# Kernel tuning notes

Measured on AMD Instinct MI355X. Metric: run time of the kernel, lower is better.

## Reference

```python
import jax, jax.numpy as jnp
import numpy as np

K = 16            # neighbors
RATIO = 0.25      # sampling ratio
BN_EPS = 1e-5


def setup_inputs() -> dict:
    key = jax.random.key(0)
    k1, k2, k3 = jax.random.split(key, 3)
    B, N, Cin, Cout = 8, 8192, 64, 128
    x = jax.random.normal(k1, (B, N, Cin), dtype=jnp.float32)
    p1 = jax.random.uniform(k2, (B, N, 3), dtype=jnp.float32)
    W = jax.random.normal(k3, (Cout, Cin), dtype=jnp.float32) * 0.05  # Conv1d(k=1, bias=False)
    gamma = jnp.ones((Cout,), dtype=jnp.float32)   # BatchNorm1d weight
    beta = jnp.zeros((Cout,), dtype=jnp.float32)   # BatchNorm1d bias
    return {"x": x, "p1": p1, "W": W, "gamma": gamma, "beta": beta}


def furthest_point_sample(p, M):
    """Greedy FPS. p: (B,N,3) -> (B,M) int32 indices. Starts at index 0 (CUDA impl convention)."""
    B, N, _ = p.shape
    first = jnp.zeros((B,), dtype=jnp.int32)
    mind = jnp.full((B, N), 1e10, dtype=p.dtype)

    def step(carry, _):
        mind, last = carry
        lp = jnp.take_along_axis(p, last[:, None, None].astype(jnp.int32), axis=1)  # (B,1,3)
        d = jnp.sum((p - lp) ** 2, axis=-1)          # (B,N)
        mind = jnp.minimum(mind, d)
        nxt = jnp.argmax(mind, axis=1).astype(jnp.int32)
        return (mind, nxt), nxt

    (_, _), rest = jax.lax.scan(step, (mind, first), None, length=M - 1)  # rest: (M-1,B)
    idx = jnp.concatenate([first[None, :], rest], axis=0)  # (M,B)
    return idx.T  # (B,M)


def reference(x, p1, W, gamma, beta):
    B, N, Cin = x.shape
    M = int(N * RATIO)

    # --- FPS sampling + gather coords ---
    fps_idx = furthest_point_sample(p1, M)                      # (B,M)
    p2 = jnp.take_along_axis(p1, fps_idx[:, :, None], axis=1)   # (B,M,3)

    # --- brute-force kNN of p1 around each p2 query ---
    d2 = (jnp.sum(p2 ** 2, -1)[:, :, None]
          - 2.0 * jnp.einsum('bmd,bnd->bmn', p2, p1)
          + jnp.sum(p1 ** 2, -1)[:, None, :])                   # (B,M,N)
    _, nbr = jax.lax.top_k(-d2, K)                              # (B,M,K) indices into N

    # --- shared MLP: 1x1 conv (no bias) + BatchNorm1d (training-mode stats) + ReLU ---
    h = jnp.einsum('bnc,oc->bno', x, W)                         # (B,N,Cout)
    mean = jnp.mean(h, axis=(0, 1))
    var = jnp.var(h, axis=(0, 1))
    h = (h - mean) * jax.lax.rsqrt(var + BN_EPS) * gamma + beta
    h = jax.nn.relu(h)

    # --- gather k neighbors per sampled point, max-pool over neighborhood ---
    feats = h[jnp.arange(B)[:, None, None], nbr]                # (B,M,K,Cout)
    y = jnp.max(feats, axis=2)                                  # (B,M,Cout)
    return y, p2
```

## Files before the change

kernel.cpp:

```cpp
#include <hip/hip_runtime.h>
#include <stdint.h>

#define Bb   8
#define Nn   8192
#define CIN  64
#define COUT 128
#define Mm   2048
#define KNN  16
#define NTOT (Bb*Nn)

typedef unsigned long long ull;
typedef float v2f __attribute__((ext_vector_type(2)));

#define MAGIC 0x55AA1234u


__device__ __forceinline__ v2f pk_add(v2f a, v2f b)
{ v2f d; asm("v_pk_add_f32 %0, %1, %2" : "=v"(d) : "v"(a), "v"(b)); return d; }
__device__ __forceinline__ v2f pk_mul(v2f a, v2f b)
{ v2f d; asm("v_pk_mul_f32 %0, %1, %2" : "=v"(d) : "v"(a), "v"(b)); return d; }

__device__ __forceinline__ float wave_max16(float x)
{
    int v = __float_as_int(x), t;
    t = __builtin_amdgcn_update_dpp(v, v, 0x111, 0xf, 0xf, false);
    v = __float_as_int(fmaxf(__int_as_float(v), __int_as_float(t)));
    t = __builtin_amdgcn_update_dpp(v, v, 0x112, 0xf, 0xf, false);
    v = __float_as_int(fmaxf(__int_as_float(v), __int_as_float(t)));
    t = __builtin_amdgcn_update_dpp(v, v, 0x114, 0xf, 0xf, false);
    v = __float_as_int(fmaxf(__int_as_float(v), __int_as_float(t)));
    t = __builtin_amdgcn_update_dpp(v, v, 0x118, 0xf, 0xf, false);
    v = __float_as_int(fmaxf(__int_as_float(v), __int_as_float(t)));
    unsigned r0 = (unsigned)__builtin_amdgcn_readlane(v, 15);
    unsigned r1 = (unsigned)__builtin_amdgcn_readlane(v, 31);
    unsigned r2 = (unsigned)__builtin_amdgcn_readlane(v, 47);
    unsigned r3 = (unsigned)__builtin_amdgcn_readlane(v, 63);
    unsigned m0 = r0 > r1 ? r0 : r1;
    unsigned m1 = r2 > r3 ? r2 : r3;
    unsigned mm = m0 > m1 ? m0 : m1;
    return __uint_as_float(mm);
}

__device__ __forceinline__ ull d2key(
    float qx, float qy, float qz, float qn, float x, float y, float z, int j)
{
    float dot = __fadd_rn(__fadd_rn(__fmul_rn(qx, x), __fmul_rn(qy, y)),
                          __fmul_rn(qz, z));
    float cn  = __fadd_rn(__fadd_rn(__fmul_rn(x, x), __fmul_rn(y, y)),
                          __fmul_rn(z, z));
    float d2  = __fadd_rn(__fsub_rn(qn, __fadd_rn(dot, dot)), cn);
    unsigned int bits = __float_as_uint(d2);
    unsigned int u = bits ^ (((unsigned int)((int)bits >> 31)) | 0x80000000u);
    return ((ull)u << 32) | (unsigned int)j;
}

__global__ __launch_bounds__(256, 1)
void mega_kernel(const float* __restrict__ p1, float* __restrict__ p2out,
                 const float* __restrict__ h, const float* __restrict__ sb,
                 ull* idxpub, float* __restrict__ y)
{
    __shared__ float px[Nn], py[Nn], pz[Nn];
    __shared__ alignas(16) ull wkey[2][4];
    const int tid = threadIdx.x;

    if (blockIdx.x < 8) {
        const int b    = blockIdx.x;
        const int lane = tid & 63, wid = tid >> 6;
        const float* pb = p1 + b * Nn * 3;

        for (int i = tid; i < Nn * 3; i += 256) {
            float v = pb[i];
            int pt = i / 3;
            int c  = i - pt * 3;
            if (c == 0) px[pt] = v; else if (c == 1) py[pt] = v; else pz[pt] = v;
        }
        __syncthreads();

        v2f ppx[16], ppy[16], ppz[16], mind[16];
#pragma unroll
        for (int i = 0; i < 16; ++i) {
            int j0 = tid * 32 + 2 * i;
            ppx[i] = (v2f){px[j0], px[j0 + 1]};
            ppy[i] = (v2f){py[j0], py[j0 + 1]};
            ppz[i] = (v2f){pz[j0], pz[j0 + 1]};
            mind[i] = (v2f){1e10f, 1e10f};
        }

        float lx = px[0], ly = py[0], lz = pz[0];
        if (tid == 0) {
            __hip_atomic_store(&idxpub[b * Mm], ((ull)MAGIC << 32) | 0ull,
                               __ATOMIC_RELAXED, __HIP_MEMORY_SCOPE_AGENT);
            int o = (b * Mm) * 3;
            p2out[o] = lx; p2out[o + 1] = ly; p2out[o + 2] = lz;
        }

        for (int m = 1; m < Mm; ++m) {
            const int buf = m & 1;
            float nx = -lx, ny = -ly, nz = -lz;
            v2f nx2 = (v2f){nx, nx}, ny2 = (v2f){ny, ny}, nz2 = (v2f){nz, nz};
            float bv0 = -1.0f, bv1 = -1.0f; int bj0 = 0, bj1 = 1;
#pragma unroll
            for (int i = 0; i < 16; ++i) {
                v2f dx = pk_add(ppx[i], nx2);
                v2f dy = pk_add(ppy[i], ny2);
                v2f dz = pk_add(ppz[i], nz2);
                v2f s  = pk_add(pk_add(pk_mul(dx, dx), pk_mul(dy, dy)),
                                pk_mul(dz, dz));
                float m0 = fminf(mind[i].x, s.x);
                float m1 = fminf(mind[i].y, s.y);
                mind[i].x = m0; mind[i].y = m1;
                if (m0 > bv0) { bv0 = m0; bj0 = 2 * i; }
                if (m1 > bv1) { bv1 = m1; bj1 = 2 * i + 1; }
            }
            float bestv; int bestj;
            if (bv1 > bv0 || (bv1 == bv0 && bj1 < bj0)) { bestv = bv1; bestj = bj1; }
            else                                        { bestv = bv0; bestj = bj0; }
            bestj += tid * 32;

            float wv = wave_max16(bestv);
            ull tie = __ballot(bestv == wv);
            int low = __ffsll((long long)tie) - 1;
            if (lane == low) {
                wkey[buf][wid] = ((ull)__float_as_uint(wv) << 32) |
                                 (unsigned int)(~(unsigned int)bestj);
            }
            __syncthreads();

            ull k0 = wkey[buf][0], k1 = wkey[buf][1];
            ull k2 = wkey[buf][2], k3 = wkey[buf][3];
            ull k01 = k0 > k1 ? k0 : k1;
            ull k23 = k2 > k3 ? k2 : k3;
            ull fk  = k01 > k23 ? k01 : k23;
            int jw = (int)(~(unsigned int)fk);
            if (tid == 0) {
                __hip_atomic_store(&idxpub[b * Mm + m],
                                   ((ull)MAGIC << 32) | (ull)(unsigned)jw,
                                   __ATOMIC_RELAXED, __HIP_MEMORY_SCOPE_AGENT);
            }
            lx = px[jw]; ly = py[jw]; lz = pz[jw];
            if (tid == 0) {
                int o = (b * Mm + m) * 3;
                p2out[o] = lx; p2out[o + 1] = ly; p2out[o + 2] = lz;
            }
        }
        return;
    }

    const int cb = blockIdx.x - 8;
    const int b  = cb / 31;
    const int k  = cb - b * 31;
    const float* pb = p1 + b * Nn * 3;

    for (int i = tid; i < Nn * 3; i += 256) {
        float v = pb[i];
        int pt = i / 3;
        int c  = i - pt * 3;
        if (c == 0) px[pt] = v; else if (c == 1) py[pt] = v; else pz[pt] = v;
    }
    __syncthreads();

    const int w = tid >> 6, lane = tid & 63;
    const int c0 = lane * 2;
    const float s0 = sb[c0], s1 = sb[c0 + 1];
    const float bb0 = sb[128 + c0], bb1 = sb[128 + c0 + 1];
    const ull INV = ~0ull;

    for (int t = w; k + 31 * t < Mm; t += 4) {
        const int m = k + 31 * t;
        const int qrow = b * Mm + m;

        ull pv;
        for (;;) {
            pv = __hip_atomic_load(&idxpub[qrow], __ATOMIC_RELAXED,
                                   __HIP_MEMORY_SCOPE_AGENT);
            if ((unsigned)(pv >> 32) == MAGIC) break;
            __builtin_amdgcn_s_sleep(2);
        }
        const int jq = (int)(pv & 0x1FFFull);
        const float qx = px[jq], qy = py[jq], qz = pz[jq];
        const float qn = __fadd_rn(__fadd_rn(__fmul_rn(qx, qx), __fmul_rn(qy, qy)),
                                   __fmul_rn(qz, qz));

        ull k1 = INV, k2 = INV, k3 = INV;
#pragma unroll 4
        for (int i = 0; i < 128; ++i) {
            int j = lane + (i << 6);
            ull key = d2key(qx, qy, qz, qn, px[j], py[j], pz[j], j);
            bool b1 = key < k1, b2 = key < k2, b3 = key < k3;
            ull n1 = b1 ? key : k1;
            ull n2 = b1 ? k1 : (b2 ? key : k2);
            ull n3 = b2 ? k2 : (b3 ? key : k3);
            k1 = n1; k2 = n2; k3 = n3;
        }

        float a0 = -1e30f, a1 = -1e30f;
        for (int r = 0; r < KNN; ++r) {
            ull wk = k1;
#pragma unroll
            for (int off = 1; off < 64; off <<= 1) {
                ull ok = __shfl_xor(wk, off, 64);
                wk = ok < wk ? ok : wk;
            }
            const int n = (int)(unsigned int)(wk & 0xFFFFFFFFull);
            const float2 v = *(const float2*)(h + (((b << 13) + n) * COUT) + c0);
            if (k1 == wk) { k1 = k2; k2 = k3; k3 = INV; }
            if (k1 == INV) {
                for (int i = 0; i < 128; ++i) {
                    int j = lane + (i << 6);
                    ull key = d2key(qx, qy, qz, qn, px[j], py[j], pz[j], j);
                    if (key > wk) {
                        bool b1 = key < k1, b2 = key < k2, b3 = key < k3;
                        ull n1 = b1 ? key : k1;
                        ull n2 = b1 ? k1 : (b2 ? key : k2);
                        ull n3 = b2 ? k2 : (b3 ? key : k3);
                        k1 = n1; k2 = n2; k3 = n3;
                    }
                }
            }
            a0 = fmaxf(a0, fmaf(v.x, s0, bb0));
            a1 = fmaxf(a1, fmaf(v.y, s1, bb1));
        }
        a0 = fmaxf(a0, 0.0f); a1 = fmaxf(a1, 0.0f);
        *(float2*)(y + qrow * COUT + c0) = make_float2(a0, a1);
    }
}

__global__ __launch_bounds__(256)
void gemm_kernel(const float* __restrict__ x, const float* __restrict__ W,
                 float* __restrict__ h)
{
    const int r0 = blockIdx.x * 16 + (threadIdx.x >> 6) * 4;
    const int cp = threadIdx.x & 63;
    const float4* xp = (const float4*)(x + r0 * CIN);
    const float4* w0 = (const float4*)(W + (cp * 2) * CIN);
    const float4* w1 = (const float4*)(W + (cp * 2 + 1) * CIN);
    float a[4][2];
#pragma unroll
    for (int r = 0; r < 4; ++r) { a[r][0] = 0.f; a[r][1] = 0.f; }
#pragma unroll
    for (int k = 0; k < CIN / 4; ++k) {
        float4 wa = w0[k], wb = w1[k];
#pragma unroll
        for (int r = 0; r < 4; ++r) {
            float4 xv = xp[r * 16 + k];
            a[r][0] = fmaf(xv.x, wa.x, fmaf(xv.y, wa.y, fmaf(xv.z, wa.z, fmaf(xv.w, wa.w, a[r][0]))));
            a[r][1] = fmaf(xv.x, wb.x, fmaf(xv.y, wb.y, fmaf(xv.z, wb.z, fmaf(xv.w, wb.w, a[r][1]))));
        }
    }
#pragma unroll
    for (int r = 0; r < 4; ++r)
        *(float2*)(h + (r0 + r) * COUT + cp * 2) = make_float2(a[r][0], a[r][1]);
}

__global__ __launch_bounds__(256)
void stats_kernel(const float* __restrict__ h, float* __restrict__ stats)
{
    __shared__ float4 rs[256], rq[256];
    const int tid  = threadIdx.x;
    const int c4   = (tid & 31) * 4;
    const int rsub = tid >> 5;
    const int rbase = blockIdx.x * 256;
    float4 s = make_float4(0, 0, 0, 0), q = make_float4(0, 0, 0, 0);
    for (int i = 0; i < 32; ++i) {
        int r = rbase + rsub + i * 8;
        float4 v = *(const float4*)(h + r * COUT + c4);
        s.x += v.x; s.y += v.y; s.z += v.z; s.w += v.w;
        q.x = fmaf(v.x, v.x, q.x); q.y = fmaf(v.y, v.y, q.y);
        q.z = fmaf(v.z, v.z, q.z); q.w = fmaf(v.w, v.w, q.w);
    }
    rs[tid] = s; rq[tid] = q;
    __syncthreads();
    if (tid < 32) {
        for (int j = 1; j < 8; ++j) {
            float4 o = rs[tid + 32 * j];
            s.x += o.x; s.y += o.y; s.z += o.z; s.w += o.w;
            float4 oq = rq[tid + 32 * j];
            q.x += oq.x; q.y += oq.y; q.z += oq.z; q.w += oq.w;
        }
        atomicAdd(&stats[c4 + 0], s.x); atomicAdd(&stats[c4 + 1], s.y);
        atomicAdd(&stats[c4 + 2], s.z); atomicAdd(&stats[c4 + 3], s.w);
        atomicAdd(&stats[128 + c4 + 0], q.x); atomicAdd(&stats[128 + c4 + 1], q.y);
        atomicAdd(&stats[128 + c4 + 2], q.z); atomicAdd(&stats[128 + c4 + 3], q.w);
    }
}

__global__ void finalize_kernel(const float* __restrict__ stats,
                                const float* __restrict__ gamma,
                                const float* __restrict__ beta,
                                float* __restrict__ sb)
{
    int c = threadIdx.x;
    float mean = stats[c] * (1.0f / 65536.0f);
    float var  = stats[128 + c] * (1.0f / 65536.0f) - mean * mean;
    float scale = gamma[c] / sqrtf(var + 1e-5f);
    float bias  = beta[c] - mean * scale;
    sb[c] = scale; sb[128 + c] = bias;
}

extern "C" void kernel_launch(void* const* d_in, const int* in_sizes, int n_in,
                              void* d_out, int out_size, void* d_ws, size_t ws_size,
                              hipStream_t stream)
{
    const float* x     = (const float*)d_in[0];
    const float* p1    = (const float*)d_in[1];
    const float* W     = (const float*)d_in[2];
    const float* gamma = (const float*)d_in[3];
    const float* beta  = (const float*)d_in[4];

    float* y  = (float*)d_out;
    float* p2 = (float*)d_out + Bb * Mm * COUT;

    char*  ws     = (char*)d_ws;
    float* h      = (float*)ws;
    ull*   idxpub = (ull*)(ws + 33619968);
    float* stats  = (float*)(ws + 35717120);
    float* sb     = (float*)(ws + 35718144);

    hipMemsetAsync(stats, 0, 1024, stream);
    gemm_kernel<<<NTOT / 16, 256, 0, stream>>>(x, W, h);
    stats_kernel<<<256, 256, 0, stream>>>(h, stats);
    finalize_kernel<<<1, 128, 0, stream>>>(stats, gamma, beta, sb);
    mega_kernel<<<256, 256, 0, stream>>>(p1, p2, h, sb, idxpub, y);
}
```

Before: 2.097 ms.

## Fuse GEMM, BN stats and finalize into persistent mega kernel; double block size

Moves the 1x1-conv GEMM and the BatchNorm statistics into the consumer blocks of the persistent mega kernel, where they run while the FPS blocks start sampling. A grid-wide atomic counter barrier makes those blocks wait until all statistics are accumulated. Block size goes from 256 to 512 threads, so each FPS thread handles 16 points instead of 32 and the kNN blocks run 8 waves. This removes three kernel launches and the serial GEMM+stats prefix ahead of FPS. In exchange it relies on all 256 blocks being co-resident for the spin barrier, and the wider FPS block has a larger cross-wave reduction on every step.

```diff
diff --git a/kernel.cpp b/kernel.cpp
--- a/kernel.cpp
+++ b/kernel.cpp
@@ -8,6 +8,7 @@
 #define Mm   2048
 #define KNN  16
 #define NTOT (Bb*Nn)
+#define NCONS 248
 
 typedef unsigned long long ull;
 typedef float v2f __attribute__((ext_vector_type(2)));
@@ -54,21 +55,23 @@
     return ((ull)u << 32) | (unsigned int)j;
 }
 
-__global__ __launch_bounds__(256, 1)
+__global__ __launch_bounds__(512, 1)
 void mega_kernel(const float* __restrict__ p1, float* __restrict__ p2out,
-                 const float* __restrict__ h, const float* __restrict__ sb,
-                 ull* idxpub, float* __restrict__ y)
+                 const float* __restrict__ x, const float* __restrict__ W,
+                 const float* __restrict__ gamma, const float* __restrict__ beta,
+                 float* __restrict__ h, float* __restrict__ stats,
+                 unsigned int* done, ull* idxpub, float* __restrict__ y)
 {
     __shared__ float px[Nn], py[Nn], pz[Nn];
-    __shared__ alignas(16) ull wkey[2][4];
+    __shared__ alignas(16) ull wkey[2][8];
     const int tid = threadIdx.x;
+    const int w = tid >> 6, lane = tid & 63;
 
     if (blockIdx.x < 8) {
-        const int b    = blockIdx.x;
-        const int lane = tid & 63, wid = tid >> 6;
+        const int b = blockIdx.x;
         const float* pb = p1 + b * Nn * 3;
 
-        for (int i = tid; i < Nn * 3; i += 256) {
+        for (int i = tid; i < Nn * 3; i += 512) {
             float v = pb[i];
             int pt = i / 3;
             int c  = i - pt * 3;
@@ -76,10 +79,10 @@
         }
         __syncthreads();
 
-        v2f ppx[16], ppy[16], ppz[16], mind[16];
-#pragma unroll
-        for (int i = 0; i < 16; ++i) {
-            int j0 = tid * 32 + 2 * i;
+        v2f ppx[8], ppy[8], ppz[8], mind[8];
+#pragma unroll
+        for (int i = 0; i < 8; ++i) {
+            int j0 = tid * 16 + 2 * i;
             ppx[i] = (v2f){px[j0], px[j0 + 1]};
             ppy[i] = (v2f){py[j0], py[j0 + 1]};
             ppz[i] = (v2f){pz[j0], pz[j0 + 1]};
@@ -100,7 +103,7 @@
             v2f nx2 = (v2f){nx, nx}, ny2 = (v2f){ny, ny}, nz2 = (v2f){nz, nz};
             float bv0 = -1.0f, bv1 = -1.0f; int bj0 = 0, bj1 = 1;
 #pragma unroll
-            for (int i = 0; i < 16; ++i) {
+            for (int i = 0; i < 8; ++i) {
                 v2f dx = pk_add(ppx[i], nx2);
                 v2f dy = pk_add(ppy[i], ny2);
                 v2f dz = pk_add(ppz[i], nz2);
@@ -115,22 +118,20 @@
             float bestv; int bestj;
             if (bv1 > bv0 || (bv1 == bv0 && bj1 < bj0)) { bestv = bv1; bestj = bj1; }
             else                                        { bestv = bv0; bestj = bj0; }
-            bestj += tid * 32;
+            bestj += tid * 16;
 
             float wv = wave_max16(bestv);
             ull tie = __ballot(bestv == wv);
             int low = __ffsll((long long)tie) - 1;
             if (lane == low) {
-                wkey[buf][wid] = ((ull)__float_as_uint(wv) << 32) |
-                                 (unsigned int)(~(unsigned int)bestj);
+                wkey[buf][w] = ((ull)__float_as_uint(wv) << 32) |
+                               (unsigned int)(~(unsigned int)bestj);
             }
             __syncthreads();
 
-            ull k0 = wkey[buf][0], k1 = wkey[buf][1];
-            ull k2 = wkey[buf][2], k3 = wkey[buf][3];
-            ull k01 = k0 > k1 ? k0 : k1;
-            ull k23 = k2 > k3 ? k2 : k3;
-            ull fk  = k01 > k23 ? k01 : k23;
+            ull fk = wkey[buf][0];
+#pragma unroll
+            for (int q = 1; q < 8; ++q) { ull k = wkey[buf][q]; fk = k > fk ? k : fk; }
             int jw = (int)(~(unsigned int)fk);
             if (tid == 0) {
                 __hip_atomic_store(&idxpub[b * Mm + m],
@@ -147,11 +148,74 @@
     }
 
     const int cb = blockIdx.x - 8;
-    const int b  = cb / 31;
-    const int k  = cb - b * 31;
+    const int cp = lane;
+    {
+        const float4* w0 = (const float4*)(W + (cp * 2) * CIN);
+        const float4* w1 = (const float4*)(W + (cp * 2 + 1) * CIN);
+        float s0 = 0.f, s1 = 0.f, q0 = 0.f, q1 = 0.f;
+        for (int r0 = cb * 32 + w * 4; r0 < NTOT; r0 += NCONS * 32) {
+            const float4* xp = (const float4*)(x + r0 * CIN);
+            float a[4][2];
+#pragma unroll
+            for (int r = 0; r < 4; ++r) { a[r][0] = 0.f; a[r][1] = 0.f; }
+#pragma unroll
+            for (int k = 0; k < CIN / 4; ++k) {
+                float4 wa = w0[k], wb = w1[k];
+#pragma unroll
+                for (int r = 0; r < 4; ++r) {
+                    float4 xv = xp[r * 16 + k];
+                    a[r][0] = fmaf(xv.x, wa.x, fmaf(xv.y, wa.y, fmaf(xv.z, wa.z, fmaf(xv.w, wa.w, a[r][0]))));
+                    a[r][1] = fmaf(xv.x, wb.x, fmaf(xv.y, wb.y, fmaf(xv.z, wb.z, fmaf(xv.w, wb.w, a[r][1]))));
+                }
+            }
+#pragma unroll
+            for (int r = 0; r < 4; ++r) {
+                *(float2*)(h + (r0 + r) * COUT + cp * 2) = make_float2(a[r][0], a[r][1]);
+                s0 += a[r][0]; s1 += a[r][1];
+                q0 = fmaf(a[r][0], a[r][0], q0); q1 = fmaf(a[r][1], a[r][1], q1);
+            }
+        }
+        float4* comb = (float4*)px;
+        comb[w * 64 + cp] = make_float4(s0, s1, q0, q1);
+        __syncthreads();
+        if (tid < 64) {
+            float4 t = comb[cp];
+#pragma unroll
+            for (int j = 1; j < 8; ++j) {
+                float4 o = comb[j * 64 + cp];
+                t.x += o.x; t.y += o.y; t.z += o.z; t.w += o.w;
+            }
+            atomicAdd(&stats[2 * cp], t.x);     atomicAdd(&stats[2 * cp + 1], t.y);
+            atomicAdd(&stats[128 + 2 * cp], t.z); atomicAdd(&stats[128 + 2 * cp + 1], t.w);
+        }
+        __syncthreads();
+        if (tid == 0) {
+            __hip_atomic_fetch_add(done, 1u, __ATOMIC_RELEASE,
+                                   __HIP_MEMORY_SCOPE_AGENT);
+            while (__hip_atomic_load(done, __ATOMIC_ACQUIRE,
+                                     __HIP_MEMORY_SCOPE_AGENT) < NCONS)
+                __builtin_amdgcn_s_sleep(2);
+        }
+        __syncthreads();
+    }
+
+    float sc0, sc1, bi0, bi1;
+    {
+        float mean0 = stats[2 * cp] * (1.0f / 65536.0f);
+        float mean1 = stats[2 * cp + 1] * (1.0f / 65536.0f);
+        float var0  = stats[128 + 2 * cp] * (1.0f / 65536.0f) - mean0 * mean0;
+        float var1  = stats[128 + 2 * cp + 1] * (1.0f / 65536.0f) - mean1 * mean1;
+        sc0 = gamma[2 * cp] / sqrtf(var0 + 1e-5f);
+        sc1 = gamma[2 * cp + 1] / sqrtf(var1 + 1e-5f);
+        bi0 = beta[2 * cp] - mean0 * sc0;
+        bi1 = beta[2 * cp + 1] - mean1 * sc1;
+    }
+
+    const int b = cb / 31;
+    const int k = cb - b * 31;
     const float* pb = p1 + b * Nn * 3;
 
-    for (int i = tid; i < Nn * 3; i += 256) {
+    for (int i = tid; i < Nn * 3; i += 512) {
         float v = pb[i];
         int pt = i / 3;
         int c  = i - pt * 3;
@@ -159,13 +223,10 @@
     }
     __syncthreads();
 
-    const int w = tid >> 6, lane = tid & 63;
     const int c0 = lane * 2;
-    const float s0 = sb[c0], s1 = sb[c0 + 1];
-    const float bb0 = sb[128 + c0], bb1 = sb[128 + c0 + 1];
     const ull INV = ~0ull;
 
-    for (int t = w; k + 31 * t < Mm; t += 4) {
+    for (int t = w; k + 31 * t < Mm; t += 8) {
         const int m = k + 31 * t;
         const int qrow = b * Mm + m;
 
@@ -217,84 +278,12 @@
                     }
                 }
             }
-            a0 = fmaxf(a0, fmaf(v.x, s0, bb0));
-            a1 = fmaxf(a1, fmaf(v.y, s1, bb1));
+            a0 = fmaxf(a0, fmaf(v.x, sc0, bi0));
+            a1 = fmaxf(a1, fmaf(v.y, sc1, bi1));
         }
         a0 = fmaxf(a0, 0.0f); a1 = fmaxf(a1, 0.0f);
         *(float2*)(y + qrow * COUT + c0) = make_float2(a0, a1);
     }
-}
-
-__global__ __launch_bounds__(256)
-void gemm_kernel(const float* __restrict__ x, const float* __restrict__ W,
-                 float* __restrict__ h)
-{
-    const int r0 = blockIdx.x * 16 + (threadIdx.x >> 6) * 4;
-    const int cp = threadIdx.x & 63;
-    const float4* xp = (const float4*)(x + r0 * CIN);
-    const float4* w0 = (const float4*)(W + (cp * 2) * CIN);
-    const float4* w1 = (const float4*)(W + (cp * 2 + 1) * CIN);
-    float a[4][2];
-#pragma unroll
-    for (int r = 0; r < 4; ++r) { a[r][0] = 0.f; a[r][1] = 0.f; }
-#pragma unroll
-    for (int k = 0; k < CIN / 4; ++k) {
-        float4 wa = w0[k], wb = w1[k];
-#pragma unroll
-        for (int r = 0; r < 4; ++r) {
-            float4 xv = xp[r * 16 + k];
-            a[r][0] = fmaf(xv.x, wa.x, fmaf(xv.y, wa.y, fmaf(xv.z, wa.z, fmaf(xv.w, wa.w, a[r][0]))));
-            a[r][1] = fmaf(xv.x, wb.x, fmaf(xv.y, wb.y, fmaf(xv.z, wb.z, fmaf(xv.w, wb.w, a[r][1]))));
-        }
-    }
-#pragma unroll
-    for (int r = 0; r < 4; ++r)
-        *(float2*)(h + (r0 + r) * COUT + cp * 2) = make_float2(a[r][0], a[r][1]);
-}
-
-__global__ __launch_bounds__(256)
-void stats_kernel(const float* __restrict__ h, float* __restrict__ stats)
-{
-    __shared__ float4 rs[256], rq[256];
-    const int tid  = threadIdx.x;
-    const int c4   = (tid & 31) * 4;
-    const int rsub = tid >> 5;
-    const int rbase = blockIdx.x * 256;
-    float4 s = make_float4(0, 0, 0, 0), q = make_float4(0, 0, 0, 0);
-    for (int i = 0; i < 32; ++i) {
-        int r = rbase + rsub + i * 8;
-        float4 v = *(const float4*)(h + r * COUT + c4);
-        s.x += v.x; s.y += v.y; s.z += v.z; s.w += v.w;
-        q.x = fmaf(v.x, v.x, q.x); q.y = fmaf(v.y, v.y, q.y);
-        q.z = fmaf(v.z, v.z, q.z); q.w = fmaf(v.w, v.w, q.w);
-    }
-    rs[tid] = s; rq[tid] = q;
-    __syncthreads();
-    if (tid < 32) {
-        for (int j = 1; j < 8; ++j) {
-            float4 o = rs[tid + 32 * j];
-            s.x += o.x; s.y += o.y; s.z += o.z; s.w += o.w;
-            float4 oq = rq[tid + 32 * j];
-            q.x += oq.x; q.y += oq.y; q.z += oq.z; q.w += oq.w;
-        }
-        atomicAdd(&stats[c4 + 0], s.x); atomicAdd(&stats[c4 + 1], s.y);
-        atomicAdd(&stats[c4 + 2], s.z); atomicAdd(&stats[c4 + 3], s.w);
-        atomicAdd(&stats[128 + c4 + 0], q.x); atomicAdd(&stats[128 + c4 + 1], q.y);
-        atomicAdd(&stats[128 + c4 + 2], q.z); atomicAdd(&stats[128 + c4 + 3], q.w);
-    }
-}
-
-__global__ void finalize_kernel(const float* __restrict__ stats,
-                                const float* __restrict__ gamma,
-                                const float* __restrict__ beta,
-                                float* __restrict__ sb)
-{
-    int c = threadIdx.x;
-    float mean = stats[c] * (1.0f / 65536.0f);
-    float var  = stats[128 + c] * (1.0f / 65536.0f) - mean * mean;
-    float scale = gamma[c] / sqrtf(var + 1e-5f);
-    float bias  = beta[c] - mean * scale;
-    sb[c] = scale; sb[128 + c] = bias;
 }
 
 extern "C" void kernel_launch(void* const* d_in, const int* in_sizes, int n_in,
@@ -314,11 +303,9 @@
     float* h      = (float*)ws;
     ull*   idxpub = (ull*)(ws + 33619968);
     float* stats  = (float*)(ws + 35717120);
-    float* sb     = (float*)(ws + 35718144);
-
-    hipMemsetAsync(stats, 0, 1024, stream);
-    gemm_kernel<<<NTOT / 16, 256, 0, stream>>>(x, W, h);
-    stats_kernel<<<256, 256, 0, stream>>>(h, stats);
-    finalize_kernel<<<1, 128, 0, stream>>>(stats, gamma, beta, sb);
-    mega_kernel<<<256, 256, 0, stream>>>(p1, p2, h, sb, idxpub, y);
+    unsigned int* done = (unsigned int*)(ws + 35718144);
+
+    hipMemsetAsync(stats, 0, 2048, stream);
+    mega_kernel<<<256, 512, 0, stream>>>(p1, p2, x, W, gamma, beta,
+                                         h, stats, done, idxpub, y);
 }
```

Measured after the change: 2.072 ms. No clear change (-1.2%).
